# Optimization experiments

Hardware: AMD Instinct MI355X
Metric: run time of the kernel (lower is better)

## Reference

```python
import jax, jax.numpy as jnp
import numpy as np

N, E = 50000, 300000
NI, EI, H, OUT, L = 16, 8, 64, 3, 3  # node/edge input widths, hidden, output, conv_depth


def setup_inputs() -> dict:
    key = jax.random.key(0)
    ks = iter(jax.random.split(key, 64))
    def rn(shape, scale=0.05):
        return jax.random.normal(next(ks), shape, dtype=jnp.float32) * scale
    inp = {}
    inp["nodes"] = jax.random.normal(next(ks), (N, NI), dtype=jnp.float32)
    inp["edges"] = jax.random.normal(next(ks), (E, EI), dtype=jnp.float32)
    inp["edge_idx"] = jax.random.randint(next(ks), (E, 2), 0, N, dtype=jnp.int32)
    def mlp_params(prefix, din, lead=None):
        s = () if lead is None else (lead,)
        inp[prefix + "_W1"] = rn(s + (din, H))
        inp[prefix + "_b1"] = jnp.zeros(s + (H,), jnp.float32)
        inp[prefix + "_W2"] = rn(s + (H, H))
        inp[prefix + "_b2"] = jnp.zeros(s + (H,), jnp.float32)
        inp[prefix + "_g"] = jnp.ones(s + (H,), jnp.float32)
        inp[prefix + "_be"] = jnp.zeros(s + (H,), jnp.float32)
    mlp_params("ne", NI)            # node encoder
    mlp_params("ee", EI)            # edge encoder
    mlp_params("nm", 2 * H, lead=L)  # node messengers (stacked over conv_depth)
    mlp_params("em", 3 * H, lead=L)  # edge messengers
    inp["dec_W1"] = rn((H, H)); inp["dec_b1"] = jnp.zeros((H,), jnp.float32)
    inp["dec_W2"] = rn((H, OUT)); inp["dec_b2"] = jnp.zeros((OUT,), jnp.float32)
    return inp


def _lrelu(x):
    return jnp.where(x >= 0, x, 0.05 * x)


def _ln(x, g, b):
    m = jnp.mean(x, axis=-1, keepdims=True)
    v = jnp.mean((x - m) ** 2, axis=-1, keepdims=True)
    return (x - m) * jax.lax.rsqrt(v + 1e-5) * g + b


def _mlp(x, W1, b1, W2, b2, g, b):
    h = _lrelu(x @ W1 + b1)
    h = _lrelu(h @ W2 + b2)
    return _ln(h, g, b)


def reference(nodes, edges, edge_idx,
              ne_W1, ne_b1, ne_W2, ne_b2, ne_g, ne_be,
              ee_W1, ee_b1, ee_W2, ee_b2, ee_g, ee_be,
              nm_W1, nm_b1, nm_W2, nm_b2, nm_g, nm_be,
              em_W1, em_b1, em_W2, em_b2, em_g, em_be,
              dec_W1, dec_b1, dec_W2, dec_b2):
    n = _mlp(nodes, ne_W1, ne_b1, ne_W2, ne_b2, ne_g, ne_be)   # [N, H]
    e = _mlp(edges, ee_W1, ee_b1, ee_W2, ee_b2, ee_g, ee_be)   # [E, H]
    s, r = edge_idx[:, 0], edge_idx[:, 1]
    for i in range(L):
        e = e + _mlp(jnp.concatenate([e, n[s], n[r]], axis=1),
                     em_W1[i], em_b1[i], em_W2[i], em_b2[i], em_g[i], em_be[i])
        aggr = jax.ops.segment_sum(e, s, num_segments=n.shape[0])  # scatter_add onto senders
        n = n + _mlp(jnp.concatenate([n, aggr], axis=1),
                     nm_W1[i], nm_b1[i], nm_W2[i], nm_b2[i], nm_g[i], nm_be[i])
    h = _lrelu(n @ dec_W1 + dec_b1)
    return h @ dec_W2 + dec_b2  # [N, OUT]
```

## Files before the change

### kernel.cpp

```cpp
#include <hip/hip_runtime.h>

constexpr int BT = 256;

typedef __attribute__((ext_vector_type(8))) short short8v;
typedef __attribute__((ext_vector_type(4))) short short4v;
typedef __attribute__((ext_vector_type(4))) float f32x4;

__device__ __forceinline__ float lrelu(float x) { return x >= 0.f ? x : 0.05f * x; }

__device__ __forceinline__ unsigned short bf16_rne(float x) {
    unsigned u = __float_as_uint(x);
    u += 0x7FFFu + ((u >> 16) & 1u);
    return (unsigned short)(u >> 16);
}
__device__ __forceinline__ float bf16_to_f(unsigned short h) {
    return __uint_as_float(((unsigned)h) << 16);
}
__device__ __forceinline__ void split2(float x, unsigned short& hi, unsigned short& lo) {
    hi = bf16_rne(x);
    lo = bf16_rne(x - bf16_to_f(hi));
}


__device__ __forceinline__ void stageA64(const float* __restrict__ src, int row0, int nrows,
                                         short* __restrict__ A)
{
    for (int q = threadIdx.x; q < 1024; q += 256) {
        const int row = q >> 4;
        const int k0 = (q & 15) << 2;
        const int grow = row0 + row;
        float4 x = (grow < nrows) ? *reinterpret_cast<const float4*>(src + (long long)grow * 64 + k0)
                                  : make_float4(0.f, 0.f, 0.f, 0.f);
        unsigned short h0,h1,h2,h3,l0,l1,l2,l3;
        split2(x.x, h0, l0); split2(x.y, h1, l1); split2(x.z, h2, l2); split2(x.w, h3, l3);
        const int off = row * 64 + ((((k0 >> 3) ^ (row & 7))) << 3) + (k0 & 7);
        short4v hv; hv[0]=(short)h0; hv[1]=(short)h1; hv[2]=(short)h2; hv[3]=(short)h3;
        short4v lv; lv[0]=(short)l0; lv[1]=(short)l1; lv[2]=(short)l2; lv[3]=(short)l3;
        *reinterpret_cast<short4v*>(A + off) = hv;
        *reinterpret_cast<short4v*>(A + 4096 + off) = lv;
    }
}

__device__ __forceinline__ void gemm64(const short* __restrict__ A, const short* __restrict__ wf,
                                       int row, int g, int lane, f32x4* __restrict__ acc)
{
    #pragma unroll
    for (int s = 0; s < 2; ++s) {
        const int k8 = s * 4 + g;
        const int aoff = row * 64 + ((k8 ^ (row & 7)) << 3);
        const short8v a_hi = *reinterpret_cast<const short8v*>(A + aoff);
        const short8v a_lo = *reinterpret_cast<const short8v*>(A + 4096 + aoff);
        #pragma unroll
        for (int t = 0; t < 4; ++t) {
            const short8v b_hi = *reinterpret_cast<const short8v*>(wf + ((s*4+t)*2+0)*512 + lane*8);
            const short8v b_lo = *reinterpret_cast<const short8v*>(wf + ((s*4+t)*2+1)*512 + lane*8);
            acc[t] = __builtin_amdgcn_mfma_f32_16x16x32_bf16(a_hi, b_hi, acc[t], 0, 0, 0);
            acc[t] = __builtin_amdgcn_mfma_f32_16x16x32_bf16(a_lo, b_hi, acc[t], 0, 0, 0);
            acc[t] = __builtin_amdgcn_mfma_f32_16x16x32_bf16(a_hi, b_lo, acc[t], 0, 0, 0);
        }
    }
}

__global__ void k_prepw(const float* __restrict__ emW1, const float* __restrict__ emW2,
                        const float* __restrict__ nmW1, const float* __restrict__ nmW2,
                        const float* __restrict__ eeW2, const float* __restrict__ neW2,
                        const float* __restrict__ decW1,
                        short* __restrict__ wf)
{
    const int cid = blockIdx.x;
    const float* src;
    if (cid < 21) {
        const int layer = cid / 7, j = cid % 7;
        src =
            j == 0 ? emW1 + (size_t)layer * 12288 :
            j == 1 ? emW1 + (size_t)layer * 12288 + 4096 :
            j == 2 ? emW1 + (size_t)layer * 12288 + 8192 :
            j == 3 ? emW2 + (size_t)layer * 4096 :
            j == 4 ? nmW1 + (size_t)layer * 8192 :
            j == 5 ? nmW1 + (size_t)layer * 8192 + 4096 :
                     nmW2 + (size_t)layer * 4096;
    } else {
        src = (cid == 21) ? eeW2 : (cid == 22) ? neW2 : decW1;
    }
    short* dst = wf + (size_t)cid * 8192;
    for (int fr = threadIdx.x; fr < 1024; fr += 256) {
        const int lane = fr & 63;
        const int stp = fr >> 6;
        const int p = stp & 1;
        const int st = stp >> 1;
        const int s = st >> 2, t = st & 3;
        const int col = t * 16 + (lane & 15);
        const int k0 = s * 32 + (lane >> 4) * 8;
        short8v o;
        #pragma unroll
        for (int i = 0; i < 8; ++i) {
            const float w = src[(k0 + i) * 64 + col];
            const unsigned short hi = bf16_rne(w);
            o[i] = (short)(p ? bf16_rne(w - bf16_to_f(hi)) : hi);
        }
        *reinterpret_cast<short8v*>(dst + fr * 8) = o;
    }
}

template<int DIN, bool PERM>
__global__ __launch_bounds__(256) void k_enc_mf(
    const float* __restrict__ x, const int* __restrict__ csr,
    const float* __restrict__ W1, const float* __restrict__ b1,
    const short* __restrict__ wfW2, const float* __restrict__ b2,
    const float* __restrict__ gam, const float* __restrict__ bet,
    float* __restrict__ out, int nrows)
{
    __shared__ short Hf[8192];
    const int row0 = blockIdx.x * 64;
    const int lane = threadIdx.x & 63;
    const int wm = threadIdx.x >> 6;
    const int g = lane >> 4, c = lane & 15;
    const int rowA = wm * 16 + c;

    long long orig[4];
    #pragma unroll
    for (int r = 0; r < 4; ++r) {
        const int grow = row0 + wm * 16 + g * 4 + r;
        orig[r] = (grow < nrows) ? (long long)(PERM ? csr[grow] : grow) : -1;
    }

    const f32x4 z4 = {0.f, 0.f, 0.f, 0.f};
    f32x4 acc[4];
    #pragma unroll
    for (int t = 0; t < 4; ++t) acc[t] = z4;

    #pragma unroll
    for (int kq = 0; kq < DIN / 4; ++kq) {
        float xv[4][4];
        #pragma unroll
        for (int r = 0; r < 4; ++r) {
            float4 t4 = make_float4(0.f, 0.f, 0.f, 0.f);
            if (orig[r] >= 0)
                t4 = *reinterpret_cast<const float4*>(x + orig[r] * DIN + kq * 4);
            xv[r][0] = t4.x; xv[r][1] = t4.y; xv[r][2] = t4.z; xv[r][3] = t4.w;
        }
        #pragma unroll
        for (int i = 0; i < 4; ++i) {
            const int k = kq * 4 + i;
            float wv[4];
            #pragma unroll
            for (int t = 0; t < 4; ++t) wv[t] = W1[k * 64 + t * 16 + c];
            #pragma unroll
            for (int t = 0; t < 4; ++t)
                #pragma unroll
                for (int r = 0; r < 4; ++r)
                    acc[t][r] = fmaf(xv[r][i], wv[t], acc[t][r]);
        }
    }

    #pragma unroll
    for (int t = 0; t < 4; ++t) {
        const int col = t * 16 + c;
        const float b1v = b1[col];
        #pragma unroll
        for (int r = 0; r < 4; ++r) {
            const int rl = wm * 16 + g * 4 + r;
            const float h = lrelu(acc[t][r] + b1v);
            unsigned short hi, lo; split2(h, hi, lo);
            const int off = rl * 64 + (((col >> 3) ^ (rl & 7)) << 3) + (col & 7);
            Hf[off] = (short)hi;
            Hf[4096 + off] = (short)lo;
        }
    }

    f32x4 acc2[4];
    #pragma unroll
    for (int t = 0; t < 4; ++t) acc2[t] = z4;
    gemm64(Hf, wfW2, rowA, g, lane, acc2);

    #pragma unroll
    for (int t = 0; t < 4; ++t) {
        const float b2v = b2[t * 16 + c];
        #pragma unroll
        for (int r = 0; r < 4; ++r) acc2[t][r] = lrelu(acc2[t][r] + b2v);
    }
    float gv[4], bv[4];
    #pragma unroll
    for (int t = 0; t < 4; ++t) { gv[t] = gam[t * 16 + c]; bv[t] = bet[t * 16 + c]; }
    #pragma unroll
    for (int r = 0; r < 4; ++r) {
        float s = acc2[0][r] + acc2[1][r] + acc2[2][r] + acc2[3][r];
        s += __shfl_xor(s, 1); s += __shfl_xor(s, 2); s += __shfl_xor(s, 4); s += __shfl_xor(s, 8);
        const float mu = s * 0.015625f;
        float q = 0.f;
        #pragma unroll
        for (int t = 0; t < 4; ++t) { const float d = acc2[t][r] - mu; q = fmaf(d, d, q); }
        q += __shfl_xor(q, 1); q += __shfl_xor(q, 2); q += __shfl_xor(q, 4); q += __shfl_xor(q, 8);
        const float rs = rsqrtf(q * 0.015625f + 1e-5f);
        const int grow = row0 + wm * 16 + g * 4 + r;
        if (grow < nrows) {
            #pragma unroll
            for (int t = 0; t < 4; ++t)
                out[(long long)grow * 64 + t * 16 + c] = (acc2[t][r] - mu) * rs * gv[t] + bv[t];
        }
    }
}

__global__ __launch_bounds__(256) void k_uv_mf(
    const float* __restrict__ n, const short* __restrict__ wfB, const short* __restrict__ wfC,
    float* __restrict__ u, float* __restrict__ v, int N)
{
    __shared__ short Ab[8192];
    const int row0 = blockIdx.x * 64;
    stageA64(n, row0, N, Ab);
    __syncthreads();
    const int lane = threadIdx.x & 63;
    const int wm = threadIdx.x >> 6;
    const int g = lane >> 4, c = lane & 15;
    const int rowA = wm * 16 + c;
    const f32x4 z4 = {0.f, 0.f, 0.f, 0.f};
    f32x4 acc[4];
    #pragma unroll
    for (int t = 0; t < 4; ++t) acc[t] = z4;
    gemm64(Ab, wfB, rowA, g, lane, acc);
    #pragma unroll
    for (int r = 0; r < 4; ++r) {
        const int grow = row0 + wm * 16 + g * 4 + r;
        if (grow < N) {
            #pragma unroll
            for (int t = 0; t < 4; ++t) u[(long long)grow * 64 + t * 16 + c] = acc[t][r];
        }
    }
    #pragma unroll
    for (int t = 0; t < 4; ++t) acc[t] = z4;
    gemm64(Ab, wfC, rowA, g, lane, acc);
    #pragma unroll
    for (int r = 0; r < 4; ++r) {
        const int grow = row0 + wm * 16 + g * 4 + r;
        if (grow < N) {
            #pragma unroll
            for (int t = 0; t < 4; ++t) v[(long long)grow * 64 + t * 16 + c] = acc[t][r];
        }
    }
}

__global__ __launch_bounds__(256) void k_edge_mf(
    float* __restrict__ e, const int* __restrict__ sp, const int* __restrict__ rp,
    const float* __restrict__ u, const float* __restrict__ v,
    const short* __restrict__ wfA, const short* __restrict__ wfW2,
    const float* __restrict__ b1, const float* __restrict__ b2,
    const float* __restrict__ gam, const float* __restrict__ bet, int E)
{
    __shared__ short Ab[8192];
    __shared__ short Hf[8192];
    const int row0 = blockIdx.x * 64;
    stageA64(e, row0, E, Ab);
    __syncthreads();
    const int lane = threadIdx.x & 63;
    const int wm = threadIdx.x >> 6;
    const int g = lane >> 4, c = lane & 15;
    const int rowA = wm * 16 + c;
    int sidx[4], ridx[4];
    #pragma unroll
    for (int r = 0; r < 4; ++r) {
        const int grow = row0 + wm * 16 + g * 4 + r;
        if (grow < E) { sidx[r] = sp[grow]; ridx[r] = rp[grow]; }
        else          { sidx[r] = 0; ridx[r] = 0; }
    }
    const f32x4 z4 = {0.f, 0.f, 0.f, 0.f};
    f32x4 acc[4];
    #pragma unroll
    for (int t = 0; t < 4; ++t) acc[t] = z4;
    gemm64(Ab, wfA, rowA, g, lane, acc);
    #pragma unroll
    for (int t = 0; t < 4; ++t) {
        const int col = t * 16 + c;
        const float b1v = b1[col];
        #pragma unroll
        for (int r = 0; r < 4; ++r)
            acc[t][r] += b1v + u[(long long)sidx[r] * 64 + col] + v[(long long)ridx[r] * 64 + col];
    }
    #pragma unroll
    for (int t = 0; t < 4; ++t) {
        const int col = t * 16 + c;
        #pragma unroll
        for (int r = 0; r < 4; ++r) {
            const int rl = wm * 16 + g * 4 + r;
            const float h = lrelu(acc[t][r]);
            unsigned short hi, lo; split2(h, hi, lo);
            const int off = rl * 64 + (((col >> 3) ^ (rl & 7)) << 3) + (col & 7);
            Hf[off] = (short)hi;
            Hf[4096 + off] = (short)lo;
        }
    }
    f32x4 acc2[4];
    #pragma unroll
    for (int t = 0; t < 4; ++t) acc2[t] = z4;
    gemm64(Hf, wfW2, rowA, g, lane, acc2);
    #pragma unroll
    for (int t = 0; t < 4; ++t) {
        const float b2v = b2[t * 16 + c];
        #pragma unroll
        for (int r = 0; r < 4; ++r) acc2[t][r] = lrelu(acc2[t][r] + b2v);
    }
    float gv[4], bv[4];
    #pragma unroll
    for (int t = 0; t < 4; ++t) { gv[t] = gam[t * 16 + c]; bv[t] = bet[t * 16 + c]; }
    #pragma unroll
    for (int r = 0; r < 4; ++r) {
        float s = acc2[0][r] + acc2[1][r] + acc2[2][r] + acc2[3][r];
        s += __shfl_xor(s, 1); s += __shfl_xor(s, 2); s += __shfl_xor(s, 4); s += __shfl_xor(s, 8);
        const float mu = s * 0.015625f;
        float q = 0.f;
        #pragma unroll
        for (int t = 0; t < 4; ++t) { const float d = acc2[t][r] - mu; q = fmaf(d, d, q); }
        q += __shfl_xor(q, 1); q += __shfl_xor(q, 2); q += __shfl_xor(q, 4); q += __shfl_xor(q, 8);
        const float rs = rsqrtf(q * 0.015625f + 1e-5f);
        const int rl = wm * 16 + g * 4 + r;
        const int grow = row0 + rl;
        if (grow < E) {
            #pragma unroll
            for (int t = 0; t < 4; ++t) {
                const int col = t * 16 + c;
                const int off = rl * 64 + (((col >> 3) ^ (rl & 7)) << 3) + (col & 7);
                const float eo = bf16_to_f((unsigned short)Ab[off]) + bf16_to_f((unsigned short)Ab[4096 + off]);
                e[(long long)grow * 64 + col] = (acc2[t][r] - mu) * rs * gv[t] + bv[t] + eo;
            }
        }
    }
}

__global__ __launch_bounds__(256) void k_node_mf(
    float* __restrict__ n, const float* __restrict__ aggr,
    const short* __restrict__ wfW1a, const short* __restrict__ wfW1b, const short* __restrict__ wfW2,
    const float* __restrict__ b1, const float* __restrict__ b2,
    const float* __restrict__ gam, const float* __restrict__ bet, int N)
{
    __shared__ short An[8192];
    __shared__ short Aa[8192];
    __shared__ short Hf[8192];
    const int row0 = blockIdx.x * 64;
    stageA64(n, row0, N, An);
    stageA64(aggr, row0, N, Aa);
    __syncthreads();
    const int lane = threadIdx.x & 63;
    const int wm = threadIdx.x >> 6;
    const int g = lane >> 4, c = lane & 15;
    const int rowA = wm * 16 + c;
    const f32x4 z4 = {0.f, 0.f, 0.f, 0.f};
    f32x4 acc[4];
    #pragma unroll
    for (int t = 0; t < 4; ++t) acc[t] = z4;
    gemm64(An, wfW1a, rowA, g, lane, acc);
    gemm64(Aa, wfW1b, rowA, g, lane, acc);
    #pragma unroll
    for (int t = 0; t < 4; ++t) {
        const int col = t * 16 + c;
        const float b1v = b1[col];
        #pragma unroll
        for (int r = 0; r < 4; ++r) {
            const int rl = wm * 16 + g * 4 + r;
            const float h = lrelu(acc[t][r] + b1v);
            unsigned short hi, lo; split2(h, hi, lo);
            const int off = rl * 64 + (((col >> 3) ^ (rl & 7)) << 3) + (col & 7);
            Hf[off] = (short)hi;
            Hf[4096 + off] = (short)lo;
        }
    }
    f32x4 acc2[4];
    #pragma unroll
    for (int t = 0; t < 4; ++t) acc2[t] = z4;
    gemm64(Hf, wfW2, rowA, g, lane, acc2);
    #pragma unroll
    for (int t = 0; t < 4; ++t) {
        const float b2v = b2[t * 16 + c];
        #pragma unroll
        for (int r = 0; r < 4; ++r) acc2[t][r] = lrelu(acc2[t][r] + b2v);
    }
    float gv[4], bv[4];
    #pragma unroll
    for (int t = 0; t < 4; ++t) { gv[t] = gam[t * 16 + c]; bv[t] = bet[t * 16 + c]; }
    #pragma unroll
    for (int r = 0; r < 4; ++r) {
        float s = acc2[0][r] + acc2[1][r] + acc2[2][r] + acc2[3][r];
        s += __shfl_xor(s, 1); s += __shfl_xor(s, 2); s += __shfl_xor(s, 4); s += __shfl_xor(s, 8);
        const float mu = s * 0.015625f;
        float q = 0.f;
        #pragma unroll
        for (int t = 0; t < 4; ++t) { const float d = acc2[t][r] - mu; q = fmaf(d, d, q); }
        q += __shfl_xor(q, 1); q += __shfl_xor(q, 2); q += __shfl_xor(q, 4); q += __shfl_xor(q, 8);
        const float rs = rsqrtf(q * 0.015625f + 1e-5f);
        const int rl = wm * 16 + g * 4 + r;
        const int grow = row0 + rl;
        if (grow < N) {
            #pragma unroll
            for (int t = 0; t < 4; ++t) {
                const int col = t * 16 + c;
                const int off = rl * 64 + (((col >> 3) ^ (rl & 7)) << 3) + (col & 7);
                const float no = bf16_to_f((unsigned short)An[off]) + bf16_to_f((unsigned short)An[4096 + off]);
                n[(long long)grow * 64 + col] = (acc2[t][r] - mu) * rs * gv[t] + bv[t] + no;
            }
        }
    }
}

__global__ __launch_bounds__(256) void k_dec_mf(
    const float* __restrict__ n, const short* __restrict__ wfW1, const float* __restrict__ b1,
    const float* __restrict__ W2, const float* __restrict__ b2,
    float* __restrict__ out, int N)
{
    __shared__ short An[8192];
    __shared__ float hrow[4096];
    const int row0 = blockIdx.x * 64;
    stageA64(n, row0, N, An);
    __syncthreads();
    const int lane = threadIdx.x & 63;
    const int wm = threadIdx.x >> 6;
    const int g = lane >> 4, c = lane & 15;
    const int rowA = wm * 16 + c;
    const f32x4 z4 = {0.f, 0.f, 0.f, 0.f};
    f32x4 acc[4];
    #pragma unroll
    for (int t = 0; t < 4; ++t) acc[t] = z4;
    gemm64(An, wfW1, rowA, g, lane, acc);
    #pragma unroll
    for (int t = 0; t < 4; ++t) {
        const int col = t * 16 + c;
        const float b1v = b1[col];
        #pragma unroll
        for (int r = 0; r < 4; ++r) {
            const int rl = wm * 16 + g * 4 + r;
            hrow[rl * 64 + (col ^ (rl & 31))] = lrelu(acc[t][r] + b1v);
        }
    }
    __syncthreads();
    const int row = threadIdx.x >> 2, o = threadIdx.x & 3;
    if (o < 3 && row0 + row < N) {
        float s = b2[o];
        #pragma unroll 8
        for (int k = 0; k < 64; ++k)
            s = fmaf(hrow[row * 64 + (k ^ (row & 31))], W2[k * 3 + o], s);
        out[(long long)(row0 + row) * 3 + o] = s;
    }
}

__global__ void k_hist(const int* __restrict__ eidx, int* __restrict__ cnt, int E)
{
    int i = blockIdx.x * 256 + threadIdx.x;
    if (i < E) atomicAdd(&cnt[eidx[2 * i]], 1);
}

__global__ void k_scan1(const int* __restrict__ cnt, int* __restrict__ starts,
                        int* __restrict__ bsum, int n)
{
    __shared__ int sh[256];
    const int tid = threadIdx.x;
    const int i = blockIdx.x * 256 + tid;
    const int val = (i < n) ? cnt[i] : 0;
    sh[tid] = val; __syncthreads();
    for (int off = 1; off < 256; off <<= 1) {
        int t = (tid >= off) ? sh[tid - off] : 0;
        __syncthreads();
        sh[tid] += t;
        __syncthreads();
    }
    if (i < n) starts[i] = sh[tid] - val;
    if (tid == 255) bsum[blockIdx.x] = sh[255];
}

__global__ void k_scan2(int* __restrict__ bsum, int nb)
{
    __shared__ int sh[256];
    const int tid = threadIdx.x;
    const int val = (tid < nb) ? bsum[tid] : 0;
    sh[tid] = val; __syncthreads();
    for (int off = 1; off < 256; off <<= 1) {
        int t = (tid >= off) ? sh[tid - off] : 0;
        __syncthreads();
        sh[tid] += t;
        __syncthreads();
    }
    if (tid < nb) bsum[tid] = sh[tid] - val;
}

__global__ void k_scan3(int* __restrict__ starts, const int* __restrict__ bsum, int n)
{
    int i = blockIdx.x * 256 + threadIdx.x;
    if (i < n) starts[i] += bsum[blockIdx.x];
}

__global__ void k_scatter(const int* __restrict__ eidx, const int* __restrict__ starts,
                          int* __restrict__ cursor, int* __restrict__ csr,
                          int* __restrict__ sp, int* __restrict__ rp, int E)
{
    int i = blockIdx.x * 256 + threadIdx.x;
    if (i < E) {
        const int s = eidx[2 * i];
        const int p = atomicAdd(&cursor[s], 1);
        const int q = starts[s] + p;
        csr[q] = i;
        sp[q] = s;
        rp[q] = eidx[2 * i + 1];
    }
}

__global__ __launch_bounds__(256) void k_aggr(
    const float* __restrict__ e, const int* __restrict__ starts, const int* __restrict__ cnt,
    float* __restrict__ aggr, int N)
{
    const int node = blockIdx.x * 4 + (threadIdx.x >> 6);
    if (node >= N) return;
    const int j = threadIdx.x & 63;
    const int st = starts[node], en = st + cnt[node];
    float a = 0.f;
    for (int t = st; t < en; ++t)
        a += e[(long long)t * 64 + j];
    aggr[(long long)node * 64 + j] = a;
}

extern "C" void kernel_launch(void* const* d_in, const int* in_sizes, int n_in,
                              void* d_out, int out_size, void* d_ws, size_t ws_size,
                              hipStream_t stream)
{
    (void)in_sizes; (void)n_in; (void)out_size; (void)ws_size;
    constexpr int N = 50000, E = 300000, L = 3;

    const float* nodes = (const float*)d_in[0];
    const float* edges = (const float*)d_in[1];
    const int*   eidx  = (const int*)d_in[2];
    const float* neW1 = (const float*)d_in[3];
    const float* neb1 = (const float*)d_in[4];
    const float* neW2 = (const float*)d_in[5];
    const float* neb2 = (const float*)d_in[6];
    const float* neg  = (const float*)d_in[7];
    const float* nebe = (const float*)d_in[8];
    const float* eeW1 = (const float*)d_in[9];
    const float* eeb1 = (const float*)d_in[10];
    const float* eeW2 = (const float*)d_in[11];
    const float* eeb2 = (const float*)d_in[12];
    const float* eeg  = (const float*)d_in[13];
    const float* eebe = (const float*)d_in[14];
    const float* nmW1 = (const float*)d_in[15];
    const float* nmb1 = (const float*)d_in[16];
    const float* nmW2 = (const float*)d_in[17];
    const float* nmb2 = (const float*)d_in[18];
    const float* nmg  = (const float*)d_in[19];
    const float* nmbe = (const float*)d_in[20];
    const float* emW1 = (const float*)d_in[21];
    const float* emb1 = (const float*)d_in[22];
    const float* emW2 = (const float*)d_in[23];
    const float* emb2 = (const float*)d_in[24];
    const float* emg  = (const float*)d_in[25];
    const float* embe = (const float*)d_in[26];
    const float* decW1 = (const float*)d_in[27];
    const float* decb1 = (const float*)d_in[28];
    const float* decW2 = (const float*)d_in[29];
    const float* decb2 = (const float*)d_in[30];

    float* n   = (float*)d_ws;
    float* u   = n + (size_t)N * 64;
    float* v   = u + (size_t)N * 64;
    float* e   = v + (size_t)N * 64;
    int* cnt    = (int*)(e + (size_t)E * 64);
    int* starts = cnt + N;
    int* csr    = starts + N;
    int* bsum   = csr + E;
    int* cursor = bsum + 256;
    int* sp     = cursor + N;
    int* rp     = sp + E;
    short* wf   = (short*)(rp + E);

    const int nbN = (N + BT - 1) / BT;
    const int nbE = (E + BT - 1) / BT;
    const int nbN64 = (N + 63) / 64;
    const int nbE64 = (E + 63) / 64;

    const short* wfEE  = wf + (size_t)21 * 8192;
    const short* wfNE  = wf + (size_t)22 * 8192;
    const short* wfDec = wf + (size_t)23 * 8192;

    k_prepw<<<24, 256, 0, stream>>>(emW1, emW2, nmW1, nmW2, eeW2, neW2, decW1, wf);
    hipMemsetAsync(cnt, 0, (size_t)N * sizeof(int), stream);
    hipMemsetAsync(cursor, 0, (size_t)N * sizeof(int), stream);
    k_hist<<<nbE, 256, 0, stream>>>(eidx, cnt, E);
    k_scan1<<<nbN, 256, 0, stream>>>(cnt, starts, bsum, N);
    k_scan2<<<1, 256, 0, stream>>>(bsum, nbN);
    k_scan3<<<nbN, 256, 0, stream>>>(starts, bsum, N);
    k_scatter<<<nbE, 256, 0, stream>>>(eidx, starts, cursor, csr, sp, rp, E);

    k_enc_mf<16, false><<<nbN64, 256, 0, stream>>>(nodes, nullptr, neW1, neb1, wfNE,
                                                   neb2, neg, nebe, n, N);
    k_enc_mf<8, true><<<nbE64, 256, 0, stream>>>(edges, csr, eeW1, eeb1, wfEE,
                                                 eeb2, eeg, eebe, e, E);

    for (int i = 0; i < L; ++i) {
        const short* wl = wf + (size_t)i * 7 * 8192;
        k_uv_mf<<<nbN64, 256, 0, stream>>>(n, wl + 8192, wl + 2 * 8192, u, v, N);
        k_edge_mf<<<nbE64, 256, 0, stream>>>(e, sp, rp, u, v, wl, wl + 3 * 8192,
                                             emb1 + i * 64, emb2 + i * 64,
                                             emg + i * 64, embe + i * 64, E);
        k_aggr<<<(N + 3) / 4, 256, 0, stream>>>(e, starts, cnt, u, N);
        k_node_mf<<<nbN64, 256, 0, stream>>>(n, u, wl + 4 * 8192, wl + 5 * 8192, wl + 6 * 8192,
                                             nmb1 + i * 64, nmb2 + i * 64,
                                             nmg + i * 64, nmbe + i * 64, N);
    }
    k_dec_mf<<<nbN64, 256, 0, stream>>>(n, wfDec, decb1, decW2, decb2, (float*)d_out, N);
}
```

Measured before the change: 455.5 us.

## Permute MFMA output column mapping so each lane owns four contiguous columns

The pre-packed weight fragments now map each lane's output column to c*4+t instead of t*16+c. Each lane then holds four adjacent output columns per row. That lets bias, gamma/beta, the u/v gathers, the LDS writes of the hidden activations and the global stores all use float4/short4 vector accesses instead of scalar ones. The risk is a correctness dependence on every consumer agreeing on the new column permutation, and LDS bank patterns change under the swizzle.

Result: no change. 462.0 us (+1.4%).

```diff
diff --git a/kernel.cpp b/kernel.cpp
--- a/kernel.cpp
+++ b/kernel.cpp
@@ -89,7 +89,7 @@
         const int p = stp & 1;
         const int st = stp >> 1;
         const int s = st >> 2, t = st & 3;
-        const int col = t * 16 + (lane & 15);
+        const int col = ((lane & 15) << 2) + t;
         const int k0 = s * 32 + (lane >> 4) * 8;
         short8v o;
         #pragma unroll
@@ -115,6 +115,7 @@
     const int lane = threadIdx.x & 63;
     const int wm = threadIdx.x >> 6;
     const int g = lane >> 4, c = lane & 15;
+    const int c4 = c << 2;
     const int rowA = wm * 16 + c;
 
     long long orig[4];
@@ -142,9 +143,8 @@
         #pragma unroll
         for (int i = 0; i < 4; ++i) {
             const int k = kq * 4 + i;
-            float wv[4];
-            #pragma unroll
-            for (int t = 0; t < 4; ++t) wv[t] = W1[k * 64 + t * 16 + c];
+            const float4 w4 = *reinterpret_cast<const float4*>(W1 + k * 64 + c4);
+            const float wv[4] = {w4.x, w4.y, w4.z, w4.w};
             #pragma unroll
             for (int t = 0; t < 4; ++t)
                 #pragma unroll
@@ -153,19 +153,21 @@
         }
     }
 
-    #pragma unroll
-    for (int t = 0; t < 4; ++t) {
-        const int col = t * 16 + c;
-        const float b1v = b1[col];
-        #pragma unroll
-        for (int r = 0; r < 4; ++r) {
-            const int rl = wm * 16 + g * 4 + r;
-            const float h = lrelu(acc[t][r] + b1v);
+    const float4 b1q = *reinterpret_cast<const float4*>(b1 + c4);
+    const float b1a[4] = {b1q.x, b1q.y, b1q.z, b1q.w};
+    #pragma unroll
+    for (int r = 0; r < 4; ++r) {
+        const int rl = wm * 16 + g * 4 + r;
+        const int off = rl * 64 + (((c4 >> 3) ^ (rl & 7)) << 3) + (c4 & 7);
+        short4v hv, lv;
+        #pragma unroll
+        for (int t = 0; t < 4; ++t) {
+            const float h = lrelu(acc[t][r] + b1a[t]);
             unsigned short hi, lo; split2(h, hi, lo);
-            const int off = rl * 64 + (((col >> 3) ^ (rl & 7)) << 3) + (col & 7);
-            Hf[off] = (short)hi;
-            Hf[4096 + off] = (short)lo;
-        }
+            hv[t] = (short)hi; lv[t] = (short)lo;
+        }
+        *reinterpret_cast<short4v*>(Hf + off) = hv;
+        *reinterpret_cast<short4v*>(Hf + 4096 + off) = lv;
     }
 
     f32x4 acc2[4];
@@ -173,15 +175,17 @@
     for (int t = 0; t < 4; ++t) acc2[t] = z4;
     gemm64(Hf, wfW2, rowA, g, lane, acc2);
 
+    const float4 b2q = *reinterpret_cast<const float4*>(b2 + c4);
+    const float b2a[4] = {b2q.x, b2q.y, b2q.z, b2q.w};
     #pragma unroll
     for (int t = 0; t < 4; ++t) {
-        const float b2v = b2[t * 16 + c];
-        #pragma unroll
-        for (int r = 0; r < 4; ++r) acc2[t][r] = lrelu(acc2[t][r] + b2v);
-    }
-    float gv[4], bv[4];
-    #pragma unroll
-    for (int t = 0; t < 4; ++t) { gv[t] = gam[t * 16 + c]; bv[t] = bet[t * 16 + c]; }
+        #pragma unroll
+        for (int r = 0; r < 4; ++r) acc2[t][r] = lrelu(acc2[t][r] + b2a[t]);
+    }
+    const float4 gq = *reinterpret_cast<const float4*>(gam + c4);
+    const float4 bq = *reinterpret_cast<const float4*>(bet + c4);
+    const float gv[4] = {gq.x, gq.y, gq.z, gq.w};
+    const float bv[4] = {bq.x, bq.y, bq.z, bq.w};
     #pragma unroll
     for (int r = 0; r < 4; ++r) {
         float s = acc2[0][r] + acc2[1][r] + acc2[2][r] + acc2[3][r];
@@ -194,9 +198,12 @@
         const float rs = rsqrtf(q * 0.015625f + 1e-5f);
         const int grow = row0 + wm * 16 + g * 4 + r;
         if (grow < nrows) {
-            #pragma unroll
-            for (int t = 0; t < 4; ++t)
-                out[(long long)grow * 64 + t * 16 + c] = (acc2[t][r] - mu) * rs * gv[t] + bv[t];
+            float4 o;
+            o.x = (acc2[0][r] - mu) * rs * gv[0] + bv[0];
+            o.y = (acc2[1][r] - mu) * rs * gv[1] + bv[1];
+            o.z = (acc2[2][r] - mu) * rs * gv[2] + bv[2];
+            o.w = (acc2[3][r] - mu) * rs * gv[3] + bv[3];
+            *reinterpret_cast<float4*>(out + (long long)grow * 64 + c4) = o;
         }
     }
 }
@@ -212,6 +219,7 @@
     const int lane = threadIdx.x & 63;
     const int wm = threadIdx.x >> 6;
     const int g = lane >> 4, c = lane & 15;
+    const int c4 = c << 2;
     const int rowA = wm * 16 + c;
     const f32x4 z4 = {0.f, 0.f, 0.f, 0.f};
     f32x4 acc[4];
@@ -222,8 +230,8 @@
     for (int r = 0; r < 4; ++r) {
         const int grow = row0 + wm * 16 + g * 4 + r;
         if (grow < N) {
-            #pragma unroll
-            for (int t = 0; t < 4; ++t) u[(long long)grow * 64 + t * 16 + c] = acc[t][r];
+            float4 o; o.x = acc[0][r]; o.y = acc[1][r]; o.z = acc[2][r]; o.w = acc[3][r];
+            *reinterpret_cast<float4*>(u + (long long)grow * 64 + c4) = o;
         }
     }
     #pragma unroll
@@ -233,8 +241,8 @@
     for (int r = 0; r < 4; ++r) {
         const int grow = row0 + wm * 16 + g * 4 + r;
         if (grow < N) {
-            #pragma unroll
-            for (int t = 0; t < 4; ++t) v[(long long)grow * 64 + t * 16 + c] = acc[t][r];
+            float4 o; o.x = acc[0][r]; o.y = acc[1][r]; o.z = acc[2][r]; o.w = acc[3][r];
+            *reinterpret_cast<float4*>(v + (long long)grow * 64 + c4) = o;
         }
     }
 }
@@ -254,6 +262,7 @@
     const int lane = threadIdx.x & 63;
     const int wm = threadIdx.x >> 6;
     const int g = lane >> 4, c = lane & 15;
+    const int c4 = c << 2;
     const int rowA = wm * 16 + c;
     int sidx[4], ridx[4];
     #pragma unroll
@@ -267,40 +276,47 @@
     #pragma unroll
     for (int t = 0; t < 4; ++t) acc[t] = z4;
     gemm64(Ab, wfA, rowA, g, lane, acc);
-    #pragma unroll
-    for (int t = 0; t < 4; ++t) {
-        const int col = t * 16 + c;
-        const float b1v = b1[col];
-        #pragma unroll
-        for (int r = 0; r < 4; ++r)
-            acc[t][r] += b1v + u[(long long)sidx[r] * 64 + col] + v[(long long)ridx[r] * 64 + col];
-    }
-    #pragma unroll
-    for (int t = 0; t < 4; ++t) {
-        const int col = t * 16 + c;
-        #pragma unroll
-        for (int r = 0; r < 4; ++r) {
-            const int rl = wm * 16 + g * 4 + r;
+
+    const float4 b1q = *reinterpret_cast<const float4*>(b1 + c4);
+    #pragma unroll
+    for (int r = 0; r < 4; ++r) {
+        const float4 uu = *reinterpret_cast<const float4*>(u + (long long)sidx[r] * 64 + c4);
+        const float4 vv = *reinterpret_cast<const float4*>(v + (long long)ridx[r] * 64 + c4);
+        acc[0][r] += b1q.x + uu.x + vv.x;
+        acc[1][r] += b1q.y + uu.y + vv.y;
+        acc[2][r] += b1q.z + uu.z + vv.z;
+        acc[3][r] += b1q.w + uu.w + vv.w;
+    }
+    #pragma unroll
+    for (int r = 0; r < 4; ++r) {
+        const int rl = wm * 16 + g * 4 + r;
+        const int off = rl * 64 + (((c4 >> 3) ^ (rl & 7)) << 3) + (c4 & 7);
+        short4v hv, lv;
+        #pragma unroll
+        for (int t = 0; t < 4; ++t) {
             const float h = lrelu(acc[t][r]);
             unsigned short hi, lo; split2(h, hi, lo);
-            const int off = rl * 64 + (((col >> 3) ^ (rl & 7)) << 3) + (col & 7);
-            Hf[off] = (short)hi;
-            Hf[4096 + off] = (short)lo;
-        }
+            hv[t] = (short)hi; lv[t] = (short)lo;
+        }
+        *reinterpret_cast<short4v*>(Hf + off) = hv;
+        *reinterpret_cast<short4v*>(Hf + 4096 + off) = lv;
     }
     f32x4 acc2[4];
     #pragma unroll
     for (int t = 0; t < 4; ++t) acc2[t] = z4;
     gemm64(Hf, wfW2, rowA, g, lane, acc2);
+
+    const float4 b2q = *reinterpret_cast<const float4*>(b2 + c4);
+    const float b2a[4] = {b2q.x, b2q.y, b2q.z, b2q.w};
     #pragma unroll
     for (int t = 0; t < 4; ++t) {
-        const float b2v = b2[t * 16 + c];
-        #pragma unroll
-        for (int r = 0; r < 4; ++r) acc2[t][r] = lrelu(acc2[t][r] + b2v);
-    }
-    float gv[4], bv[4];
-    #pragma unroll
-    for (int t = 0; t < 4; ++t) { gv[t] = gam[t * 16 + c]; bv[t] = bet[t * 16 + c]; }
+        #pragma unroll
+        for (int r = 0; r < 4; ++r) acc2[t][r] = lrelu(acc2[t][r] + b2a[t]);
+    }
+    const float4 gq = *reinterpret_cast<const float4*>(gam + c4);
+    const float4 bq = *reinterpret_cast<const float4*>(bet + c4);
+    const float gv[4] = {gq.x, gq.y, gq.z, gq.w};
+    const float bv[4] = {bq.x, bq.y, bq.z, bq.w};
     #pragma unroll
     for (int r = 0; r < 4; ++r) {
         float s = acc2[0][r] + acc2[1][r] + acc2[2][r] + acc2[3][r];
@@ -314,13 +330,15 @@
         const int rl = wm * 16 + g * 4 + r;
         const int grow = row0 + rl;
         if (grow < E) {
-            #pragma unroll
-            for (int t = 0; t < 4; ++t) {
-                const int col = t * 16 + c;
-                const int off = rl * 64 + (((col >> 3) ^ (rl & 7)) << 3) + (col & 7);
-                const float eo = bf16_to_f((unsigned short)Ab[off]) + bf16_to_f((unsigned short)Ab[4096 + off]);
-                e[(long long)grow * 64 + col] = (acc2[t][r] - mu) * rs * gv[t] + bv[t] + eo;
-            }
+            const int off = rl * 64 + (((c4 >> 3) ^ (rl & 7)) << 3) + (c4 & 7);
+            const short4v eh = *reinterpret_cast<const short4v*>(Ab + off);
+            const short4v el = *reinterpret_cast<const short4v*>(Ab + 4096 + off);
+            float4 o;
+            o.x = (acc2[0][r] - mu) * rs * gv[0] + bv[0] + bf16_to_f((unsigned short)eh[0]) + bf16_to_f((unsigned short)el[0]);
+            o.y = (acc2[1][r] - mu) * rs * gv[1] + bv[1] + bf16_to_f((unsigned short)eh[1]) + bf16_to_f((unsigned short)el[1]);
+            o.z = (acc2[2][r] - mu) * rs * gv[2] + bv[2] + bf16_to_f((unsigned short)eh[2]) + bf16_to_f((unsigned short)el[2]);
+            o.w = (acc2[3][r] - mu) * rs * gv[3] + bv[3] + bf16_to_f((unsigned short)eh[3]) + bf16_to_f((unsigned short)el[3]);
+            *reinterpret_cast<float4*>(e + (long long)grow * 64 + c4) = o;
         }
     }
 }
@@ -341,6 +359,7 @@
     const int lane = threadIdx.x & 63;
     const int wm = threadIdx.x >> 6;
     const int g = lane >> 4, c = lane & 15;
+    const int c4 = c << 2;
     const int rowA = wm * 16 + c;
     const f32x4 z4 = {0.f, 0.f, 0.f, 0.f};
     f32x4 acc[4];
@@ -348,33 +367,39 @@
     for (int t = 0; t < 4; ++t) acc[t] = z4;
     gemm64(An, wfW1a, rowA, g, lane, acc);
     gemm64(Aa, wfW1b, rowA, g, lane, acc);
-    #pragma unroll
-    for (int t = 0; t < 4; ++t) {
-        const int col = t * 16 + c;
-        const float b1v = b1[col];
-        #pragma unroll
-        for (int r = 0; r < 4; ++r) {
-            const int rl = wm * 16 + g * 4 + r;
-            const float h = lrelu(acc[t][r] + b1v);
+
+    const float4 b1q = *reinterpret_cast<const float4*>(b1 + c4);
+    const float b1a[4] = {b1q.x, b1q.y, b1q.z, b1q.w};
+    #pragma unroll
+    for (int r = 0; r < 4; ++r) {
+        const int rl = wm * 16 + g * 4 + r;
+        const int off = rl * 64 + (((c4 >> 3) ^ (rl & 7)) << 3) + (c4 & 7);
+        short4v hv, lv;
+        #pragma unroll
+        for (int t = 0; t < 4; ++t) {
+            const float h = lrelu(acc[t][r] + b1a[t]);
             unsigned short hi, lo; split2(h, hi, lo);
-            const int off = rl * 64 + (((col >> 3) ^ (rl & 7)) << 3) + (col & 7);
-            Hf[off] = (short)hi;
-            Hf[4096 + off] = (short)lo;
-        }
+            hv[t] = (short)hi; lv[t] = (short)lo;
+        }
+        *reinterpret_cast<short4v*>(Hf + off) = hv;
+        *reinterpret_cast<short4v*>(Hf + 4096 + off) = lv;
     }
     f32x4 acc2[4];
     #pragma unroll
     for (int t = 0; t < 4; ++t) acc2[t] = z4;
     gemm64(Hf, wfW2, rowA, g, lane, acc2);
+
+    const float4 b2q = *reinterpret_cast<const float4*>(b2 + c4);
+    const float b2a[4] = {b2q.x, b2q.y, b2q.z, b2q.w};
     #pragma unroll
     for (int t = 0; t < 4; ++t) {
-        const float b2v = b2[t * 16 + c];
-        #pragma unroll
-        for (int r = 0; r < 4; ++r) acc2[t][r] = lrelu(acc2[t][r] + b2v);
-    }
-    float gv[4], bv[4];
-    #pragma unroll
-    for (int t = 0; t < 4; ++t) { gv[t] = gam[t * 16 + c]; bv[t] = bet[t * 16 + c]; }
+        #pragma unroll
+        for (int r = 0; r < 4; ++r) acc2[t][r] = lrelu(acc2[t][r] + b2a[t]);
+    }
+    const float4 gq = *reinterpret_cast<const float4*>(gam + c4);
+    const float4 bq = *reinterpret_cast<const float4*>(bet + c4);
+    const float gv[4] = {gq.x, gq.y, gq.z, gq.w};
+    const float bv[4] = {bq.x, bq.y, bq.z, bq.w};
     #pragma unroll
     for (int r = 0; r < 4; ++r) {
         float s = acc2[0][r] + acc2[1][r] + acc2[2][r] + acc2[3][r];
@@ -388,13 +413,15 @@
         const int rl = wm * 16 + g * 4 + r;
         const int grow = row0 + rl;
         if (grow < N) {
-            #pragma unroll
-            for (int t = 0; t < 4; ++t) {
-                const int col = t * 16 + c;
-                const int off = rl * 64 + (((col >> 3) ^ (rl & 7)) << 3) + (col & 7);
-                const float no = bf16_to_f((unsigned short)An[off]) + bf16_to_f((unsigned short)An[4096 + off]);
-                n[(long long)grow * 64 + col] = (acc2[t][r] - mu) * rs * gv[t] + bv[t] + no;
-            }
+            const int off = rl * 64 + (((c4 >> 3) ^ (rl & 7)) << 3) + (c4 & 7);
+            const short4v nh = *reinterpret_cast<const short4v*>(An + off);
+            const short4v nl = *reinterpret_cast<const short4v*>(An + 4096 + off);
+            float4 o;
+            o.x = (acc2[0][r] - mu) * rs * gv[0] + bv[0] + bf16_to_f((unsigned short)nh[0]) + bf16_to_f((unsigned short)nl[0]);
+            o.y = (acc2[1][r] - mu) * rs * gv[1] + bv[1] + bf16_to_f((unsigned short)nh[1]) + bf16_to_f((unsigned short)nl[1]);
+            o.z = (acc2[2][r] - mu) * rs * gv[2] + bv[2] + bf16_to_f((unsigned short)nh[2]) + bf16_to_f((unsigned short)nl[2]);
+            o.w = (acc2[3][r] - mu) * rs * gv[3] + bv[3] + bf16_to_f((unsigned short)nh[3]) + bf16_to_f((unsigned short)nl[3]);
+            *reinterpret_cast<float4*>(n + (long long)grow * 64 + c4) = o;
         }
     }
 }
@@ -412,20 +439,22 @@
     const int lane = threadIdx.x & 63;
     const int wm = threadIdx.x >> 6;
     const int g = lane >> 4, c = lane & 15;
+    const int c4 = c << 2;
     const int rowA = wm * 16 + c;
     const f32x4 z4 = {0.f, 0.f, 0.f, 0.f};
     f32x4 acc[4];
     #pragma unroll
     for (int t = 0; t < 4; ++t) acc[t] = z4;
     gemm64(An, wfW1, rowA, g, lane, acc);
+    const float4 b1q = *reinterpret_cast<const float4*>(b1 + c4);
+    const float b1a[4] = {b1q.x, b1q.y, b1q.z, b1q.w};
     #pragma unroll
     for (int t = 0; t < 4; ++t) {
-        const int col = t * 16 + c;
-        const float b1v = b1[col];
+        const int col = c4 + t;
         #pragma unroll
         for (int r = 0; r < 4; ++r) {
             const int rl = wm * 16 + g * 4 + r;
-            hrow[rl * 64 + (col ^ (rl & 31))] = lrelu(acc[t][r] + b1v);
+            hrow[rl * 64 + (col ^ (rl & 31))] = lrelu(acc[t][r] + b1a[t]);
         }
     }
     __syncthreads();
```
